# Optimization experiments

Hardware: AMD Instinct MI355X
Metric: run time of the kernel (lower is better)

The kernel has to match this reference:

```python
import jax, jax.numpy as jnp
import numpy as np

B, H, W, R, C = 4, 64, 64, 64, 32  # batch, height, width, in-channels r, conv out-channels


def setup_inputs() -> dict:
    key = jax.random.key(0)
    kx, kf, kg = jax.random.split(key, 3)
    x = jax.random.normal(kx, (B, H, W, R), dtype=jnp.float32)
    # 1x1 conv with in_channels=1: kernel is effectively a length-C vector
    w_f = jax.random.normal(kf, (C,), dtype=jnp.float32) * 0.1
    w_g = jax.random.normal(kg, (C,), dtype=jnp.float32) * 0.1
    gamma = jnp.ones((), dtype=jnp.float32)
    return {"x": x, "w_f": w_f, "w_g": w_g, "gamma": gamma}


def reference(x, w_f, w_g, gamma):
    b, h, w, r = x.shape
    hw = h * w
    xs = x.reshape(b, hw, r)                      # [B, HW, R]
    # conv_f / conv_g: each scalar of xs times weight vector -> [B, HW, R*C]
    x_f = (xs[..., None] * w_f).reshape(b, hw, -1)
    x_g = (xs[..., None] * w_g).reshape(b, hw, -1)
    attn = jnp.einsum('bik,bjk->bij', x_f, x_g)   # [B, HW, HW]
    attn = jax.nn.softmax(attn, axis=-1) * gamma
    # out[b,j,r] = sum_i attn[b,j,i] * xs[b,i,r]
    out = jnp.einsum('bji,bir->bjr', attn, xs)
    return out.reshape(b, h, w, r)
```

## Files before the change

kernel.cpp:

```cpp
#include <hip/hip_runtime.h>


#define N_SEQ 4096
#define KS    4
#define LOG2E 1.4426950408889634f

typedef __attribute__((ext_vector_type(8))) short short8;
typedef __attribute__((ext_vector_type(4))) short short4v;
typedef __attribute__((ext_vector_type(4))) float f4;
typedef _Float16 half8  __attribute__((ext_vector_type(8)));
typedef _Float16 half4v __attribute__((ext_vector_type(4)));
typedef _Float16 half2t __attribute__((ext_vector_type(2)));
typedef __fp16   fp16x2 __attribute__((ext_vector_type(2)));

union U8  { short8 v8; short4v v4[2]; unsigned short u[8]; };
union HU8 { half8 v; half2t h2[4]; unsigned short u[8]; };
union HU4 { half4v v; half2t h2[2]; unsigned short u[4]; };
union PK  { fp16x2 f; half2t h; };

#define MFMA16(a,b,c) __builtin_amdgcn_mfma_f32_16x16x32_bf16(a,b,c,0,0,0)
#define MFMAH(a,b,c)  __builtin_amdgcn_mfma_f32_16x16x32_f16(a,b,c,0,0,0)

static __device__ __forceinline__ unsigned short f2bf(float f){
  unsigned int u = __float_as_uint(f);
  u += 0x7fffu + ((u>>16)&1u);
  return (unsigned short)(u>>16);
}
static __device__ __forceinline__ float bf2f(unsigned short b){
  return __uint_as_float(((unsigned int)b)<<16);
}
static __device__ __forceinline__ half2t pkrtz(float a, float b){
#if __has_builtin(__builtin_amdgcn_cvt_pkrtz)
  PK u; u.f = __builtin_amdgcn_cvt_pkrtz(a, b);
  return u.h;
#else
  half2t r; r.x = (_Float16)a; r.y = (_Float16)b; return r;
#endif
}
static __device__ __forceinline__ float fexp2(float x){
#if __has_builtin(__builtin_amdgcn_exp2f)
  return __builtin_amdgcn_exp2f(x);
#else
  return exp2f(x);
#endif
}
static __device__ __forceinline__ f4 splat4(float v){ f4 r; r.x=v; r.y=v; r.z=v; r.w=v; return r; }
static __device__ __forceinline__ f4 exp2v(f4 v){
  f4 r; r.x=fexp2(v.x); r.y=fexp2(v.y); r.z=fexp2(v.z); r.w=fexp2(v.w); return r;
}
static __device__ __forceinline__ f4 max4(f4 a, f4 b){
  f4 r; r.x=fmaxf(a.x,b.x); r.y=fmaxf(a.y,b.y); r.z=fmaxf(a.z,b.z); r.w=fmaxf(a.w,b.w); return r;
}
static __device__ __forceinline__ f4 shx4(f4 v, int m){
  f4 r; r.x=__shfl_xor(v.x,m,64); r.y=__shfl_xor(v.y,m,64);
        r.z=__shfl_xor(v.z,m,64); r.w=__shfl_xor(v.w,m,64); return r;
}
static __device__ __forceinline__ void gld_lds16(const void* g, void* l){
  __builtin_amdgcn_global_load_lds(
      (const __attribute__((address_space(1))) unsigned int*)g,
      (__attribute__((address_space(3))) unsigned int*)l, 16, 0, 0);
}

__global__ __launch_bounds__(256) void prep_kernel(
    const float* __restrict__ x, unsigned short* __restrict__ xh,
    unsigned short* __restrict__ xt)
{
  __shared__ unsigned short T[64][66];
  const int tid = threadIdx.x;
  const int bb  = blockIdx.x >> 6;
  const int n0  = (blockIdx.x & 63) << 6;
  {
    const int r  = tid >> 2;
    const int c4 = tid & 3;
    const float* src = x + ((size_t)(bb*N_SEQ + n0 + r))*64 + c4*16;
    unsigned short h[16];
    #pragma unroll
    for (int i = 0; i < 4; ++i) {
      const float4 f = *(const float4*)(src + i*4);
      HU4 u; u.h2[0] = pkrtz(f.x, f.y); u.h2[1] = pkrtz(f.z, f.w);
      h[i*4+0]=u.u[0]; h[i*4+1]=u.u[1]; h[i*4+2]=u.u[2]; h[i*4+3]=u.u[3];
    }
    unsigned short* dst = xh + ((size_t)(bb*N_SEQ + n0 + r))*64 + c4*16;
    U8 u0, u1;
    #pragma unroll
    for (int j = 0; j < 8; ++j) { u0.u[j]=h[j]; u1.u[j]=h[8+j]; }
    *(short8*)dst = u0.v8; *(short8*)(dst+8) = u1.v8;
    #pragma unroll
    for (int j = 0; j < 16; ++j) T[r][c4*16+j] = h[j];
  }
  __syncthreads();
  {
    const int d = tid >> 2;
    const int g = tid & 3;
    unsigned short o[16];
    #pragma unroll
    for (int j = 0; j < 16; ++j) o[j] = T[g*16+j][d];
    unsigned short* dst = xt + ((size_t)(bb*64 + d))*N_SEQ + n0 + g*16;
    U8 u0, u1;
    #pragma unroll
    for (int j = 0; j < 8; ++j) { u0.u[j]=o[j]; u1.u[j]=o[8+j]; }
    *(short8*)dst = u0.v8; *(short8*)(dst+8) = u1.v8;
  }
}

__global__ __launch_bounds__(256, 4) void fattn4_kernel(
    const float* __restrict__ x, const float* __restrict__ wf,
    const float* __restrict__ wg,
    const unsigned short* __restrict__ xh, const unsigned short* __restrict__ xt,
    float* __restrict__ OP, float* __restrict__ LP)
{
  __shared__ __align__(16) unsigned short KH[2][4096];
  __shared__ __align__(16) unsigned short VT[2][4096];
  __shared__ __align__(16) unsigned short PB[4][1024];

  const int tid  = threadIdx.x;
  const int lane = tid & 63;
  const int wv   = tid >> 6;
  const int mg   = wv & 1;
  const int hh   = wv >> 1;
  const int quad = lane >> 4;
  const int l15  = lane & 15;
  const int swz  = l15 & 7;
  const int psw  = (l15 & 3) << 1;
  const int ks   = blockIdx.x >> 8;
  const int rem  = blockIdx.x & 255;
  const int bb   = rem >> 6;
  const int qb   = (rem & 63) << 6;

  float s = 0.f;
  #pragma unroll
  for (int i = 0; i < 32; ++i) s += wf[i]*wg[i];
  const float s2 = s * LOG2E;

  const float* xb = x + ((size_t)bb * N_SEQ) * 64;

  half8 qf[2][2];
  #pragma unroll
  for (int mt = 0; mt < 2; ++mt) {
    const int row = qb + mg*32 + mt*16 + l15;
    #pragma unroll
    for (int c = 0; c < 2; ++c) {
      const float* src = xb + row*64 + c*32 + quad*8;
      const float4 a0 = *(const float4*)src;
      const float4 a1 = *(const float4*)(src+4);
      HU8 u;
      u.h2[0] = pkrtz(a0.x*s2, a0.y*s2);
      u.h2[1] = pkrtz(a0.z*s2, a0.w*s2);
      u.h2[2] = pkrtz(a1.x*s2, a1.y*s2);
      u.h2[3] = pkrtz(a1.z*s2, a1.w*s2);
      qf[mt][c] = u.v;
    }
  }

  f4 Oc[2][4];
  f4 lsa[2];
  #pragma unroll
  for (int mt = 0; mt < 2; ++mt) {
    lsa[mt] = splat4(0.f);
    #pragma unroll
    for (int nt = 0; nt < 4; ++nt) Oc[mt][nt] = splat4(0.f);
  }

  const int kbb = ks*1024;
  unsigned short* PBw = PB[wv];

  #pragma unroll 1
  for (int t = 0; t < 8; ++t) {
    const int kt = kbb + t*64;
    #pragma unroll
    for (int i = 0; i < 8; ++i) {
      const int reg = i >> 1;
      const int h   = reg & 1;
      const int ch  = wv*2 + (i & 1);
      const int p   = ch*64 + lane;
      const int rr  = p >> 3;
      const int cg  = (p & 7) ^ (rr & 7);
      if (reg < 2) {
        gld_lds16(xh + ((size_t)(bb*N_SEQ + kt + h*512 + rr))*64 + cg*8, &KH[h][ch*512]);
      } else {
        gld_lds16(xt + ((size_t)(bb*64 + rr))*N_SEQ + (kt + h*512 + cg*8), &VT[h][ch*512]);
      }
    }
    __syncthreads();

    f4 St[4][2];
    #pragma unroll
    for (int k2 = 0; k2 < 4; ++k2)
      #pragma unroll
      for (int mt = 0; mt < 2; ++mt) St[k2][mt] = splat4(0.f);

    #pragma unroll
    for (int c = 0; c < 2; ++c) {
      half8 kf[4];
      #pragma unroll
      for (int k2 = 0; k2 < 4; ++k2)
        kf[k2] = *(const half8*)&KH[hh][(k2*16 + l15)*64 + (((c*4 + quad) ^ swz))*8];
      #pragma unroll
      for (int k2 = 0; k2 < 4; ++k2)
        #pragma unroll
        for (int mt = 0; mt < 2; ++mt)
          St[k2][mt] = MFMAH(kf[k2], qf[mt][c], St[k2][mt]);
    }

    #pragma unroll
    for (int kc = 0; kc < 2; ++kc) {
      #pragma unroll
      for (int k2l = 0; k2l < 2; ++k2l) {
        const int k2 = kc*2 + k2l;
        #pragma unroll
        for (int mt = 0; mt < 2; ++mt) {
          const f4 p = exp2v(St[k2][mt]);
          lsa[mt] += p;
          HU4 u; u.h2[0] = pkrtz(p.x, p.y); u.h2[1] = pkrtz(p.z, p.w);
          const int unit = (k2l*4 + quad) ^ psw;
          *(half4v*)&PBw[(mt*16 + l15)*32 + unit*4] = u.v;
        }
      }
      half8 pa[2];
      #pragma unroll
      for (int mt = 0; mt < 2; ++mt) {
        const int u0 = (2*quad) ^ psw;
        pa[mt] = *(const half8*)&PBw[(mt*16 + l15)*32 + u0*4];
      }
      #pragma unroll
      for (int nt = 0; nt < 4; ++nt) {
        const half8 vb = *(const half8*)&VT[hh][(nt*16 + l15)*64 + (((kc*4 + quad) ^ swz))*8];
        #pragma unroll
        for (int mt = 0; mt < 2; ++mt)
          Oc[mt][nt] = MFMAH(pa[mt], vb, Oc[mt][nt]);
      }
    }
    __syncthreads();
  }

  float lsum[2];
  #pragma unroll
  for (int mt = 0; mt < 2; ++mt) {
    float sv = lsa[mt].x + lsa[mt].y + lsa[mt].z + lsa[mt].w;
    sv += __shfl_xor(sv, 16, 64);
    sv += __shfl_xor(sv, 32, 64);
    lsum[mt] = sv;
  }

  float* MO = (float*)KH;
  float* ML = (float*)VT;
  if (hh == 1) {
    #pragma unroll
    for (int mt = 0; mt < 2; ++mt) {
      const int rbase = mg*32 + mt*16 + quad*4;
      #pragma unroll
      for (int nt = 0; nt < 4; ++nt) {
        MO[(rbase+0)*64 + nt*16 + l15] = Oc[mt][nt].x;
        MO[(rbase+1)*64 + nt*16 + l15] = Oc[mt][nt].y;
        MO[(rbase+2)*64 + nt*16 + l15] = Oc[mt][nt].z;
        MO[(rbase+3)*64 + nt*16 + l15] = Oc[mt][nt].w;
      }
      if (quad == 0) ML[mg*32 + mt*16 + l15] = lsum[mt];
    }
  }
  __syncthreads();
  if (hh == 0) {
    float* op = OP + (size_t)blockIdx.x * 4096;
    #pragma unroll
    for (int mt = 0; mt < 2; ++mt) {
      const int rbase = mg*32 + mt*16 + quad*4;
      #pragma unroll
      for (int nt = 0; nt < 4; ++nt) {
        #pragma unroll
        for (int rg = 0; rg < 4; ++rg) {
          const int rr = rbase + rg;
          op[rr*64 + nt*16 + l15] = Oc[mt][nt][rg] + MO[rr*64 + nt*16 + l15];
        }
      }
      if (quad == 0)
        LP[(size_t)blockIdx.x*64 + mg*32 + mt*16 + l15] = lsum[mt] + ML[mg*32 + mt*16 + l15];
    }
  }
}

__global__ __launch_bounds__(256) void merge_kernel(
    const float* __restrict__ OP, const float* __restrict__ LP,
    const float* __restrict__ gm, float* __restrict__ out)
{
  const int idx = blockIdx.x*256 + threadIdx.x;
  const int e0  = idx*4;
  const int d0  = e0 & 63;
  const int row = e0 >> 6;
  const int bb  = row >> 12;
  const int q   = row & 4095;
  const int qt  = q >> 6;
  const int qr  = q & 63;
  float4 acc = make_float4(0.f,0.f,0.f,0.f);
  float l = 0.f;
  #pragma unroll
  for (int sct = 0; sct < KS; ++sct) {
    const int blk = sct*256 + bb*64 + qt;
    const float4 o = *(const float4*)(OP + (size_t)blk*4096 + qr*64 + d0);
    acc.x += o.x; acc.y += o.y; acc.z += o.z; acc.w += o.w;
    l += LP[(size_t)blk*64 + qr];
  }
  const float w = gm[0] / l;
  float4 r; r.x = acc.x*w; r.y = acc.y*w; r.z = acc.z*w; r.w = acc.w*w;
  *(float4*)(out + e0) = r;
}

#define LDKF 72
#define TILEF (64*LDKF)
#define LDP 36

__global__ __launch_bounds__(256) void fattn_fallback(
    const float* __restrict__ x, const float* __restrict__ wf,
    const float* __restrict__ wg, const float* __restrict__ gm,
    float* __restrict__ out)
{
  __shared__ __align__(16) unsigned short KHI[2*TILEF];
  __shared__ __align__(16) unsigned short KLO[2*TILEF];
  __shared__ __align__(16) unsigned short VT [2*TILEF];
  __shared__ __align__(16) unsigned short PB [4*32*LDP];

  const int tid  = threadIdx.x;
  const int lane = tid & 63;
  const int wv   = tid >> 6;
  const int mg   = wv & 1;
  const int hh   = wv >> 1;
  const int quad = lane >> 4;
  const int l15  = lane & 15;
  const int bb   = blockIdx.x >> 6;
  const int qb   = (blockIdx.x & 63) << 6;

  float s = 0.f;
  #pragma unroll
  for (int i = 0; i < 32; ++i) s += wf[i]*wg[i];
  const float s2 = s * LOG2E;
  const float gamma = gm[0];

  const float* xb = x + ((size_t)bb * N_SEQ) * 64;

  short8 qhf[2][2], qlf[2][2];
  #pragma unroll
  for (int mt = 0; mt < 2; ++mt) {
    const int row = qb + mg*32 + mt*16 + l15;
    #pragma unroll
    for (int c = 0; c < 2; ++c) {
      const float* src = xb + row*64 + c*32 + quad*8;
      const float4 a0 = *(const float4*)src;
      const float4 a1 = *(const float4*)(src+4);
      float qv[8] = {a0.x,a0.y,a0.z,a0.w,a1.x,a1.y,a1.z,a1.w};
      U8 vh, vl;
      #pragma unroll
      for (int j = 0; j < 8; ++j) {
        float q = qv[j]*s2;
        unsigned short hb = f2bf(q);
        vh.u[j] = (short)hb;
        vl.u[j] = (short)f2bf(q - bf2f(hb));
      }
      qhf[mt][c] = vh.v8; qlf[mt][c] = vl.v8;
    }
  }

  f4 Oc[2][4], mo[2], ls[2];
  #pragma unroll
  for (int mt = 0; mt < 2; ++mt) {
    mo[mt] = splat4(-1e30f);
    ls[mt] = splat4(0.f);
    #pragma unroll
    for (int nt = 0; nt < 4; ++nt) Oc[mt][nt] = splat4(0.f);
  }

  const int sh   = tid >> 7;
  const int srow = (tid & 127) >> 1;
  const int sch  = tid & 1;

  float4 sr[8];
  {
    const float* sp = xb + (sh*2048 + srow)*64 + sch*32;
    #pragma unroll
    for (int i = 0; i < 8; ++i) sr[i] = *(const float4*)(sp + i*4);
    unsigned short hb[32], lb[32];
    #pragma unroll
    for (int i = 0; i < 8; ++i) {
      float vv[4] = {sr[i].x, sr[i].y, sr[i].z, sr[i].w};
      #pragma unroll
      for (int j = 0; j < 4; ++j) {
        unsigned short h = f2bf(vv[j]);
        hb[i*4+j] = h;
        lb[i*4+j] = f2bf(vv[j] - bf2f(h));
      }
    }
    const int kbase = sh*TILEF + srow*LDKF + sch*32;
    #pragma unroll
    for (int g = 0; g < 4; ++g) {
      U8 wh, wl;
      #pragma unroll
      for (int j = 0; j < 8; ++j) { wh.u[j]=(short)hb[g*8+j]; wl.u[j]=(short)lb[g*8+j]; }
      *(short8*)&KHI[kbase+g*8] = wh.v8;
      *(short8*)&KLO[kbase+g*8] = wl.v8;
    }
    #pragma unroll
    for (int j = 0; j < 32; ++j) VT[sh*TILEF + (sch*32+j)*LDKF + srow] = hb[j];
  }
  __syncthreads();

  #pragma unroll 1
  for (int t = 0; t < 32; ++t) {
    if (t+1 < 32) {
      const float* sp = xb + (sh*2048 + (t+1)*64 + srow)*64 + sch*32;
      #pragma unroll
      for (int i = 0; i < 8; ++i) sr[i] = *(const float4*)(sp + i*4);
    }

    f4 Sa[2][4];
    #pragma unroll
    for (int mt = 0; mt < 2; ++mt)
      #pragma unroll
      for (int n = 0; n < 4; ++n) Sa[mt][n] = splat4(0.f);

    const int kldsb = hh*TILEF;
    #pragma unroll
    for (int n = 0; n < 4; ++n) {
      #pragma unroll
      for (int c = 0; c < 2; ++c) {
        const int off = kldsb + (n*16 + l15)*LDKF + c*32 + quad*8;
        const short8 bh = *(const short8*)&KHI[off];
        const short8 bl = *(const short8*)&KLO[off];
        #pragma unroll
        for (int mt = 0; mt < 2; ++mt) {
          Sa[mt][n] = MFMA16(qhf[mt][c], bh, Sa[mt][n]);
          Sa[mt][n] = MFMA16(qlf[mt][c], bh, Sa[mt][n]);
          Sa[mt][n] = MFMA16(qhf[mt][c], bl, Sa[mt][n]);
        }
      }
    }

    f4 p[2][4];
    #pragma unroll
    for (int mt = 0; mt < 2; ++mt) {
      f4 rm = max4(max4(Sa[mt][0],Sa[mt][1]), max4(Sa[mt][2],Sa[mt][3]));
      rm = max4(rm, shx4(rm,1));
      rm = max4(rm, shx4(rm,2));
      rm = max4(rm, shx4(rm,4));
      rm = max4(rm, shx4(rm,8));
      f4 mn = max4(mo[mt], rm);
      f4 al = exp2v(mo[mt] - mn);
      mo[mt] = mn;
      f4 rs = splat4(0.f);
      #pragma unroll
      for (int n = 0; n < 4; ++n) { p[mt][n] = exp2v(Sa[mt][n] - mn); rs += p[mt][n]; }
      rs += shx4(rs,1); rs += shx4(rs,2); rs += shx4(rs,4); rs += shx4(rs,8);
      ls[mt] = ls[mt]*al + rs;
      #pragma unroll
      for (int nt = 0; nt < 4; ++nt) Oc[mt][nt] *= al;
    }

    const int pw = wv * (32*LDP);
    #pragma unroll
    for (int kc = 0; kc < 2; ++kc) {
      #pragma unroll
      for (int mt = 0; mt < 2; ++mt) {
        #pragma unroll
        for (int n2 = 0; n2 < 2; ++n2) {
          const f4 pv = p[mt][kc*2+n2];
          const int base = pw + (mt*16 + quad*4)*LDP + n2*16 + l15;
          ((unsigned short*)PB)[base        ] = f2bf(pv.x);
          ((unsigned short*)PB)[base +   LDP] = f2bf(pv.y);
          ((unsigned short*)PB)[base + 2*LDP] = f2bf(pv.z);
          ((unsigned short*)PB)[base + 3*LDP] = f2bf(pv.w);
        }
      }
      short8 pa[2];
      #pragma unroll
      for (int mt = 0; mt < 2; ++mt) {
        U8 u;
        const int rb = pw + (mt*16 + l15)*LDP + quad*8;
        u.v4[0] = *(const short4v*)&((unsigned short*)PB)[rb];
        u.v4[1] = *(const short4v*)&((unsigned short*)PB)[rb+4];
        pa[mt] = u.v8;
      }
      #pragma unroll
      for (int nt = 0; nt < 4; ++nt) {
        const short8 vb = *(const short8*)&VT[kldsb + (nt*16 + l15)*LDKF + kc*32 + quad*8];
        #pragma unroll
        for (int mt = 0; mt < 2; ++mt) Oc[mt][nt] = MFMA16(pa[mt], vb, Oc[mt][nt]);
      }
    }

    __syncthreads();

    if (t+1 < 32) {
      unsigned short hb[32], lb[32];
      #pragma unroll
      for (int i = 0; i < 8; ++i) {
        float vv[4] = {sr[i].x, sr[i].y, sr[i].z, sr[i].w};
        #pragma unroll
        for (int j = 0; j < 4; ++j) {
          unsigned short h = f2bf(vv[j]);
          hb[i*4+j] = h;
          lb[i*4+j] = f2bf(vv[j] - bf2f(h));
        }
      }
      const int kbase = sh*TILEF + srow*LDKF + sch*32;
      #pragma unroll
      for (int g = 0; g < 4; ++g) {
        U8 wh, wl;
        #pragma unroll
        for (int j = 0; j < 8; ++j) { wh.u[j]=(short)hb[g*8+j]; wl.u[j]=(short)lb[g*8+j]; }
        *(short8*)&KHI[kbase+g*8] = wh.v8;
        *(short8*)&KLO[kbase+g*8] = wl.v8;
      }
      #pragma unroll
      for (int j = 0; j < 32; ++j) VT[sh*TILEF + (sch*32+j)*LDKF + srow] = hb[j];
      __syncthreads();
    }
  }

  float* MO  = (float*)KHI;
  float* MML = (float*)KLO;
  if (hh == 1) {
    #pragma unroll
    for (int mt = 0; mt < 2; ++mt) {
      const int rbase = mg*32 + mt*16 + quad*4;
      #pragma unroll
      for (int nt = 0; nt < 4; ++nt) {
        MO[(rbase+0)*64 + nt*16 + l15] = Oc[mt][nt].x;
        MO[(rbase+1)*64 + nt*16 + l15] = Oc[mt][nt].y;
        MO[(rbase+2)*64 + nt*16 + l15] = Oc[mt][nt].z;
        MO[(rbase+3)*64 + nt*16 + l15] = Oc[mt][nt].w;
      }
      if (l15 == 0) {
        MML[rbase+0] = mo[mt].x; MML[rbase+1] = mo[mt].y;
        MML[rbase+2] = mo[mt].z; MML[rbase+3] = mo[mt].w;
        MML[64+rbase+0] = ls[mt].x; MML[64+rbase+1] = ls[mt].y;
        MML[64+rbase+2] = ls[mt].z; MML[64+rbase+3] = ls[mt].w;
      }
    }
  }
  __syncthreads();
  if (hh == 0) {
    #pragma unroll
    for (int mt = 0; mt < 2; ++mt) {
      const int rbase = mg*32 + mt*16 + quad*4;
      f4 m1, l1;
      m1.x = MML[rbase+0]; m1.y = MML[rbase+1]; m1.z = MML[rbase+2]; m1.w = MML[rbase+3];
      l1.x = MML[64+rbase+0]; l1.y = MML[64+rbase+1]; l1.z = MML[64+rbase+2]; l1.w = MML[64+rbase+3];
      const f4 mn = max4(mo[mt], m1);
      const f4 a0 = exp2v(mo[mt] - mn);
      const f4 a1 = exp2v(m1 - mn);
      f4 lt = ls[mt]*a0 + l1*a1;
      f4 w; w.x = gamma/lt.x; w.y = gamma/lt.y; w.z = gamma/lt.z; w.w = gamma/lt.w;
      #pragma unroll
      for (int nt = 0; nt < 4; ++nt) {
        #pragma unroll
        for (int rg = 0; rg < 4; ++rg) {
          const int rr = rbase + rg;
          const float o1 = MO[rr*64 + nt*16 + l15];
          const float val = (Oc[mt][nt][rg]*a0[rg] + o1*a1[rg]) * w[rg];
          out[((size_t)bb*N_SEQ + qb + rr)*64 + nt*16 + l15] = val;
        }
      }
    }
  }
}

extern "C" void kernel_launch(void* const* d_in, const int* in_sizes, int n_in,
                              void* d_out, int out_size, void* d_ws, size_t ws_size,
                              hipStream_t stream) {
  const float* x  = (const float*)d_in[0];
  const float* wf = (const float*)d_in[1];
  const float* wg = (const float*)d_in[2];
  const float* gm = (const float*)d_in[3];
  float* out = (float*)d_out;

  const size_t XH_OFF = 0;
  const size_t XT_OFF = 2097152;
  const size_t OP_OFF = 4194304;
  const size_t LP_OFF = OP_OFF + (size_t)KS*256*4096*4;
  const size_t NEED   = LP_OFF + (size_t)KS*256*64*4;

  if (ws_size >= NEED) {
    unsigned short* xhp = (unsigned short*)((char*)d_ws + XH_OFF);
    unsigned short* xtp = (unsigned short*)((char*)d_ws + XT_OFF);
    float* OP = (float*)((char*)d_ws + OP_OFF);
    float* LP = (float*)((char*)d_ws + LP_OFF);
    prep_kernel<<<dim3(256), dim3(256), 0, stream>>>(x, xhp, xtp);
    fattn4_kernel<<<dim3(KS*256), dim3(256), 0, stream>>>(x, wf, wg, xhp, xtp, OP, LP);
    merge_kernel<<<dim3(1024), dim3(256), 0, stream>>>(OP, LP, gm, out);
  } else {
    fattn_fallback<<<dim3(256), dim3(256), 0, stream>>>(x, wf, wg, gm, out);
  }
}
```

Baseline: 99.01 us.

## Double-buffer K/V tiles and give each wave its own query rows

Blocks now cover 128 query rows across 8 key splits, and each of the four waves owns 32 query rows over the full key range of its split. Before, waves were split into two key halves that had to be combined through LDS at the end. The K/V tile loads now go into a double buffer: the next 64-key tile is prefetched while the current one is computed, and one barrier per iteration replaces two. The goal is to hide global-to-LDS latency and drop the cross-wave reduction. In exchange, each block issues twice as many partial outputs to the workspace, and the merge kernel has more splits to sum.

```diff
diff --git a/kernel.cpp b/kernel.cpp
--- a/kernel.cpp
+++ b/kernel.cpp
@@ -2,7 +2,8 @@
 
 
 #define N_SEQ 4096
-#define KS    4
+#define KS    8
+#define NT    8
 #define LOG2E 1.4426950408889634f
 
 typedef __attribute__((ext_vector_type(8))) short short8;
@@ -103,7 +104,7 @@
   }
 }
 
-__global__ __launch_bounds__(256, 4) void fattn4_kernel(
+__global__ __launch_bounds__(256, 4) void fattn5_kernel(
     const float* __restrict__ x, const float* __restrict__ wf,
     const float* __restrict__ wg,
     const unsigned short* __restrict__ xh, const unsigned short* __restrict__ xt,
@@ -116,16 +117,14 @@
   const int tid  = threadIdx.x;
   const int lane = tid & 63;
   const int wv   = tid >> 6;
-  const int mg   = wv & 1;
-  const int hh   = wv >> 1;
   const int quad = lane >> 4;
   const int l15  = lane & 15;
   const int swz  = l15 & 7;
   const int psw  = (l15 & 3) << 1;
-  const int ks   = blockIdx.x >> 8;
-  const int rem  = blockIdx.x & 255;
-  const int bb   = rem >> 6;
-  const int qb   = (rem & 63) << 6;
+  const int ks   = blockIdx.x >> 7;
+  const int rem  = blockIdx.x & 127;
+  const int bb   = rem >> 5;
+  const int qb   = (rem & 31) << 7;
 
   float s = 0.f;
   #pragma unroll
@@ -137,7 +136,7 @@
   half8 qf[2][2];
   #pragma unroll
   for (int mt = 0; mt < 2; ++mt) {
-    const int row = qb + mg*32 + mt*16 + l15;
+    const int row = qb + wv*32 + mt*16 + l15;
     #pragma unroll
     for (int c = 0; c < 2; ++c) {
       const float* src = xb + row*64 + c*32 + quad*8;
@@ -161,27 +160,41 @@
     for (int nt = 0; nt < 4; ++nt) Oc[mt][nt] = splat4(0.f);
   }
 
-  const int kbb = ks*1024;
+  const int kt0 = ks * 512;
   unsigned short* PBw = PB[wv];
 
+  int srr[2], scg[2];
+  #pragma unroll
+  for (int j = 0; j < 2; ++j) {
+    const int p = j*256 + tid;
+    srr[j] = p >> 3;
+    scg[j] = (p & 7) ^ (srr[j] & 7);
+  }
+
+  #pragma unroll
+  for (int j = 0; j < 2; ++j) {
+    gld_lds16(xh + ((size_t)(bb*N_SEQ + kt0 + srr[j]))*64 + scg[j]*8,
+              &KH[0][(j*256 + wv*64)*8]);
+    gld_lds16(xt + ((size_t)(bb*64 + srr[j]))*N_SEQ + kt0 + scg[j]*8,
+              &VT[0][(j*256 + wv*64)*8]);
+  }
+
   #pragma unroll 1
-  for (int t = 0; t < 8; ++t) {
-    const int kt = kbb + t*64;
-    #pragma unroll
-    for (int i = 0; i < 8; ++i) {
-      const int reg = i >> 1;
-      const int h   = reg & 1;
-      const int ch  = wv*2 + (i & 1);
-      const int p   = ch*64 + lane;
-      const int rr  = p >> 3;
-      const int cg  = (p & 7) ^ (rr & 7);
-      if (reg < 2) {
-        gld_lds16(xh + ((size_t)(bb*N_SEQ + kt + h*512 + rr))*64 + cg*8, &KH[h][ch*512]);
-      } else {
-        gld_lds16(xt + ((size_t)(bb*64 + rr))*N_SEQ + (kt + h*512 + cg*8), &VT[h][ch*512]);
-      }
-    }
+  for (int t = 0; t < NT; ++t) {
     __syncthreads();
+    const int buf = t & 1;
+
+    if (t + 1 < NT) {
+      const int kt = kt0 + (t+1)*64;
+      const int nb = buf ^ 1;
+      #pragma unroll
+      for (int j = 0; j < 2; ++j) {
+        gld_lds16(xh + ((size_t)(bb*N_SEQ + kt + srr[j]))*64 + scg[j]*8,
+                  &KH[nb][(j*256 + wv*64)*8]);
+        gld_lds16(xt + ((size_t)(bb*64 + srr[j]))*N_SEQ + kt + scg[j]*8,
+                  &VT[nb][(j*256 + wv*64)*8]);
+      }
+    }
 
     f4 St[4][2];
     #pragma unroll
@@ -194,7 +207,7 @@
       half8 kf[4];
       #pragma unroll
       for (int k2 = 0; k2 < 4; ++k2)
-        kf[k2] = *(const half8*)&KH[hh][(k2*16 + l15)*64 + (((c*4 + quad) ^ swz))*8];
+        kf[k2] = *(const half8*)&KH[buf][(k2*16 + l15)*64 + (((c*4 + quad) ^ swz))*8];
       #pragma unroll
       for (int k2 = 0; k2 < 4; ++k2)
         #pragma unroll
@@ -224,13 +237,12 @@
       }
       #pragma unroll
       for (int nt = 0; nt < 4; ++nt) {
-        const half8 vb = *(const half8*)&VT[hh][(nt*16 + l15)*64 + (((kc*4 + quad) ^ swz))*8];
+        const half8 vb = *(const half8*)&VT[buf][(nt*16 + l15)*64 + (((kc*4 + quad) ^ swz))*8];
         #pragma unroll
         for (int mt = 0; mt < 2; ++mt)
           Oc[mt][nt] = MFMAH(pa[mt], vb, Oc[mt][nt]);
       }
     }
-    __syncthreads();
   }
 
   float lsum[2];
@@ -242,39 +254,19 @@
     lsum[mt] = sv;
   }
 
-  float* MO = (float*)KH;
-  float* ML = (float*)VT;
-  if (hh == 1) {
-    #pragma unroll
-    for (int mt = 0; mt < 2; ++mt) {
-      const int rbase = mg*32 + mt*16 + quad*4;
-      #pragma unroll
-      for (int nt = 0; nt < 4; ++nt) {
-        MO[(rbase+0)*64 + nt*16 + l15] = Oc[mt][nt].x;
-        MO[(rbase+1)*64 + nt*16 + l15] = Oc[mt][nt].y;
-        MO[(rbase+2)*64 + nt*16 + l15] = Oc[mt][nt].z;
-        MO[(rbase+3)*64 + nt*16 + l15] = Oc[mt][nt].w;
-      }
-      if (quad == 0) ML[mg*32 + mt*16 + l15] = lsum[mt];
-    }
-  }
-  __syncthreads();
-  if (hh == 0) {
-    float* op = OP + (size_t)blockIdx.x * 4096;
-    #pragma unroll
-    for (int mt = 0; mt < 2; ++mt) {
-      const int rbase = mg*32 + mt*16 + quad*4;
-      #pragma unroll
-      for (int nt = 0; nt < 4; ++nt) {
-        #pragma unroll
-        for (int rg = 0; rg < 4; ++rg) {
-          const int rr = rbase + rg;
-          op[rr*64 + nt*16 + l15] = Oc[mt][nt][rg] + MO[rr*64 + nt*16 + l15];
-        }
-      }
-      if (quad == 0)
-        LP[(size_t)blockIdx.x*64 + mg*32 + mt*16 + l15] = lsum[mt] + ML[mg*32 + mt*16 + l15];
-    }
+  float* op = OP + (size_t)blockIdx.x * 8192;
+  #pragma unroll
+  for (int mt = 0; mt < 2; ++mt) {
+    const int rb = wv*32 + mt*16 + quad*4;
+    #pragma unroll
+    for (int nt = 0; nt < 4; ++nt) {
+      op[(rb+0)*64 + nt*16 + l15] = Oc[mt][nt].x;
+      op[(rb+1)*64 + nt*16 + l15] = Oc[mt][nt].y;
+      op[(rb+2)*64 + nt*16 + l15] = Oc[mt][nt].z;
+      op[(rb+3)*64 + nt*16 + l15] = Oc[mt][nt].w;
+    }
+    if (quad == 0)
+      LP[(size_t)blockIdx.x*128 + wv*32 + mt*16 + l15] = lsum[mt];
   }
 }
 
@@ -288,16 +280,16 @@
   const int row = e0 >> 6;
   const int bb  = row >> 12;
   const int q   = row & 4095;
-  const int qt  = q >> 6;
-  const int qr  = q & 63;
+  const int qt  = q >> 7;
+  const int qr  = q & 127;
   float4 acc = make_float4(0.f,0.f,0.f,0.f);
   float l = 0.f;
   #pragma unroll
   for (int sct = 0; sct < KS; ++sct) {
-    const int blk = sct*256 + bb*64 + qt;
-    const float4 o = *(const float4*)(OP + (size_t)blk*4096 + qr*64 + d0);
+    const int blk = sct*128 + bb*32 + qt;
+    const float4 o = *(const float4*)(OP + (size_t)blk*8192 + qr*64 + d0);
     acc.x += o.x; acc.y += o.y; acc.z += o.z; acc.w += o.w;
-    l += LP[(size_t)blk*64 + qr];
+    l += LP[(size_t)blk*128 + qr];
   }
   const float w = gm[0] / l;
   float4 r; r.x = acc.x*w; r.y = acc.y*w; r.z = acc.z*w; r.w = acc.w*w;
@@ -573,8 +565,8 @@
   const size_t XH_OFF = 0;
   const size_t XT_OFF = 2097152;
   const size_t OP_OFF = 4194304;
-  const size_t LP_OFF = OP_OFF + (size_t)KS*256*4096*4;
-  const size_t NEED   = LP_OFF + (size_t)KS*256*64*4;
+  const size_t LP_OFF = OP_OFF + (size_t)1024*8192*4;
+  const size_t NEED   = LP_OFF + (size_t)1024*128*4;
 
   if (ws_size >= NEED) {
     unsigned short* xhp = (unsigned short*)((char*)d_ws + XH_OFF);
@@ -582,7 +574,7 @@
     float* OP = (float*)((char*)d_ws + OP_OFF);
     float* LP = (float*)((char*)d_ws + LP_OFF);
     prep_kernel<<<dim3(256), dim3(256), 0, stream>>>(x, xhp, xtp);
-    fattn4_kernel<<<dim3(KS*256), dim3(256), 0, stream>>>(x, wf, wg, xhp, xtp, OP, LP);
+    fattn5_kernel<<<dim3(KS*128), dim3(256), 0, stream>>>(x, wf, wg, xhp, xtp, OP, LP);
     merge_kernel<<<dim3(1024), dim3(256), 0, stream>>>(OP, LP, gm, out);
   } else {
     fattn_fallback<<<dim3(256), dim3(256), 0, stream>>>(x, wf, wg, gm, out);
```

New measurement: 96.26 us. -2.8%, faster.
